# Optimization experiments

Hardware: AMD Instinct MI355X
Metric: run time of the kernel (lower is better)

## Reference

```python
import jax, jax.numpy as jnp
import numpy as np

HEAD_SIZE = 256
N_EMBS = 1024
B, T = 8, 2048


def setup_inputs() -> dict:
    key = jax.random.key(0)
    kx, kq, kk, kv = jax.random.split(key, 4)
    # nn.Linear default init: U(-1/sqrt(fan_in), 1/sqrt(fan_in)); weights stored [out, in],
    # we store transposed [in, out] for x @ W.
    bound = 1.0 / np.sqrt(N_EMBS)
    x = jax.random.normal(kx, (B, T, N_EMBS), dtype=jnp.float32)
    Wq = jax.random.uniform(kq, (N_EMBS, HEAD_SIZE), dtype=jnp.float32, minval=-bound, maxval=bound)
    Wk = jax.random.uniform(kk, (N_EMBS, HEAD_SIZE), dtype=jnp.float32, minval=-bound, maxval=bound)
    Wv = jax.random.uniform(kv, (N_EMBS, HEAD_SIZE), dtype=jnp.float32, minval=-bound, maxval=bound)
    return {"x": x, "Wq": Wq, "Wk": Wk, "Wv": Wv}


def reference(x, Wq, Wk, Wv):
    # x: [B, T, C]
    Bn, Tn, C = x.shape
    Q = x @ Wq  # [B, T, H]
    K = x @ Wk
    V = x @ Wv
    scale = 1.0 / jnp.sqrt(jnp.asarray(HEAD_SIZE, dtype=x.dtype))
    w = jnp.einsum("bth,bsh->bts", Q, K) * scale  # [B, T, T]
    causal = jnp.tril(jnp.ones((Tn, Tn), dtype=bool))
    w = jnp.where(causal, w, -jnp.inf)
    w = jax.nn.softmax(w, axis=-1)
    out = jnp.einsum("bts,bsh->bth", w, V)  # [B, T, H]
    return out
```

## Files before the change

### kernel.cpp

```cpp
#include <hip/hip_runtime.h>

typedef short short8 __attribute__((ext_vector_type(8)));
typedef short short4v __attribute__((ext_vector_type(4)));
typedef float floatx4 __attribute__((ext_vector_type(4)));

#define HEAD 256
#define CDIM 1024
#define TT   2048

#define NBLK 61

#define WT_EL    0
#define QW_EL    786560
#define KW_EL    (QW_EL + 4194304)
#define VT_EL    (KW_EL + 4194304)
#define XC_EL    (VT_EL + 4194304)
#define NEED_FULL_BYTES ((size_t)(XC_EL + 16777216) * 2)

static __device__ __forceinline__ unsigned short f2bf(float f) {
    unsigned int u = __builtin_bit_cast(unsigned int, f);
    u += 0x7FFFu + ((u >> 16) & 1u);
    return (unsigned short)(u >> 16);
}
static __device__ __forceinline__ float bf2f(unsigned short h) {
    unsigned int u = ((unsigned int)h) << 16;
    return __builtin_bit_cast(float, u);
}

__device__ __forceinline__ void glds16(const void* g, void* l) {
    __builtin_amdgcn_global_load_lds(
        (const __attribute__((address_space(1))) void*)g,
        (__attribute__((address_space(3))) void*)l, 16, 0, 0);
}

__device__ __forceinline__ int probe_f32(const unsigned short* Wq, int flat_tid) {
    int lane = flat_tid & 63;
    int bad = 0;
    for (int i = lane; i < 512; i += 64)
        bad |= (((Wq[i] >> 7) & 0xFF) >= 128) ? 1 : 0;
#pragma unroll
    for (int off = 1; off < 64; off <<= 1) bad |= __shfl_xor(bad, off);
    return bad;
}

__global__ __launch_bounds__(256) void prep_kernel(
    const void* __restrict__ x, unsigned short* __restrict__ XT,
    const void* __restrict__ Wq, const void* __restrict__ Wk,
    const void* __restrict__ Wv, unsigned short* __restrict__ WtT) {
    __shared__ unsigned short tile[32][33];
    int t = threadIdx.x;
    int f = probe_f32((const unsigned short*)Wq, t);
    if (blockIdx.x < 16384) {
        int row = blockIdx.x;
        int c4  = t * 4;
        size_t si = (size_t)row * CDIM + c4;
        size_t di = (size_t)(row >> 7) * 131072 + (size_t)(c4 >> 6) * 8192
                  + (size_t)(row & 127) * 64 + (c4 & 63);
        short4v o;
        if (f) {
            floatx4 v = *(const floatx4*)((const float*)x + si);
#pragma unroll
            for (int j = 0; j < 4; j++) o[j] = (short)f2bf(v[j]);
        } else {
            o = *(const short4v*)((const unsigned short*)x + si);
        }
        *(short4v*)&XT[di] = o;
    } else {
        int wid = blockIdx.x - 16384;
        int k0 = (wid & 31) * 32;
        int n0 = (wid >> 5) * 32;
        const void* W = (n0 < 256) ? Wq : (n0 < 512) ? Wk : Wv;
        int c0 = n0 & 255;
        int tx = t & 31, ty = t >> 5;
#pragma unroll
        for (int i = 0; i < 4; i++) {
            int r = ty + 8 * i;
            size_t idx = (size_t)(k0 + r) * HEAD + c0 + tx;
            tile[r][tx] = f ? f2bf(((const float*)W)[idx])
                            : ((const unsigned short*)W)[idx];
        }
        __syncthreads();
#pragma unroll
        for (int i = 0; i < 4; i++) {
            int n = n0 + ty + 8 * i;
            int k = k0 + tx;
            WtT[(size_t)(n >> 7) * 131072 + (size_t)(k >> 6) * 8192
                + (n & 127) * 64 + (k & 63)] = tile[tx][ty + 8 * i];
        }
    }
}

__global__ __launch_bounds__(256) void gemm_qkv(
    const unsigned short* __restrict__ XT,
    const unsigned short* __restrict__ WtT,
    unsigned short* __restrict__ Q,
    unsigned short* __restrict__ K,
    unsigned short* __restrict__ VT2) {
    __shared__ __attribute__((aligned(16))) short sh[16384];

    int tid  = threadIdx.x;
    int wave = tid >> 6, lane = tid & 63, quad = lane >> 4, lq = lane & 15;
    int wm = wave >> 1, wn = wave & 1;

    int id = blockIdx.x;
    int xcd = id & 7, g = id >> 3;
    int bn = g % 6;
    int bm = (g / 6) * 8 + xcd;
    int m0 = bm * 128, n0b = bn * 128;

    int l4 = lane >> 2;
    int cswz = ((lane & 3) ^ (l4 & 3) ^ ((l4 >> 2) & 3)) * 8;
    const unsigned short* gA = XT  + (size_t)bm * 131072
                               + (size_t)(wave * 32 + l4) * 64 + cswz;
    const unsigned short* gB = WtT + (size_t)bn * 131072
                               + (size_t)(wave * 32 + l4) * 64 + cswz;
    int rdswz = ((quad ^ (lq & 3) ^ ((lq >> 2) & 3))) * 8;

    floatx4 acc[4][4];
#pragma unroll
    for (int i = 0; i < 4; i++)
#pragma unroll
        for (int j = 0; j < 4; j++)
#pragma unroll
            for (int r = 0; r < 4; r++) acc[i][j][r] = 0.f;

    {
        short* dA = sh + wave * 1024;
        short* dB = sh + 4096 + wave * 1024;
        glds16(gA, dA); glds16(gA + 1024, dA + 512);
        glds16(gB, dB); glds16(gB + 1024, dB + 512);
    }

    int cur = 0;
    for (int s = 0; s < 32; s++) {
        __syncthreads();
        if (s + 1 < 32) {
            size_t off = (size_t)((s + 1) >> 1) * 8192 + ((s + 1) & 1) * 32;
            short* dA = sh + (cur ^ 1) * 8192 + wave * 1024;
            short* dB = sh + (cur ^ 1) * 8192 + 4096 + wave * 1024;
            glds16(gA + off, dA); glds16(gA + off + 1024, dA + 512);
            glds16(gB + off, dB); glds16(gB + off + 1024, dB + 512);
        }
        short* As_ = sh + cur * 8192;
        short* Bs_ = As_ + 4096;
        short8 af[4], bfv[4];
#pragma unroll
        for (int i = 0; i < 4; i++)
            af[i] = *(short8*)&As_[(64 * wm + 16 * i + lq) * 32 + rdswz];
#pragma unroll
        for (int j = 0; j < 4; j++)
            bfv[j] = *(short8*)&Bs_[(64 * wn + 16 * j + lq) * 32 + rdswz];
#pragma unroll
        for (int i = 0; i < 4; i++)
#pragma unroll
            for (int j = 0; j < 4; j++)
                acc[i][j] = __builtin_amdgcn_mfma_f32_16x16x32_bf16(
                    af[i], bfv[j], acc[i][j], 0, 0, 0);
        cur ^= 1;
    }

    int sel = n0b >> 8;
    if (sel < 2) {
        unsigned short* outp = (sel == 0) ? Q : K;
        float scale = (sel == 0) ? 0.0625f : 1.0f;
        int cbase = n0b & 255;
#pragma unroll
        for (int i = 0; i < 4; i++)
#pragma unroll
            for (int j = 0; j < 4; j++)
#pragma unroll
                for (int r = 0; r < 4; r++) {
                    int rr = m0 + 64 * wm + 16 * i + quad * 4 + r;
                    int cc = cbase + 64 * wn + 16 * j + lq;
                    outp[(size_t)rr * HEAD + cc] = f2bf(acc[i][j][r] * scale);
                }
    } else {
        int cbase = n0b - 512;
        int batch = m0 >> 11;
        int t0 = m0 & 2047;
        unsigned short* Vb = VT2 + (size_t)batch * HEAD * TT;
#pragma unroll
        for (int h = 0; h < 2; h++) {
            __syncthreads();
            if (wn == h) {
#pragma unroll
                for (int i = 0; i < 4; i++)
#pragma unroll
                    for (int j = 0; j < 4; j++)
#pragma unroll
                        for (int r = 0; r < 4; r++) {
                            int cl = 16 * j + lq;
                            int ml = 64 * wm + 16 * i + quad * 4 + r;
                            sh[cl * 136 + ml] = (short)f2bf(acc[i][j][r]);
                        }
            }
            __syncthreads();
            int cl = tid >> 2;
            int d = cbase + 64 * h + cl;
#pragma unroll
            for (int g2 = 0; g2 < 4; g2++) {
                int ms = (tid & 3) * 8 + g2 * 32;
                short8 v = *(short8*)&sh[cl * 136 + ms];
                int st = (t0 + ms) >> 5;
                int sc = ms & 31;
                *(short8*)&Vb[(size_t)st * 8192 + d * 32 + sc] = v;
            }
        }
    }
}

__global__ __launch_bounds__(256, 2) void attn(
    const unsigned short* __restrict__ Q,
    const unsigned short* __restrict__ K,
    const unsigned short* __restrict__ VT2,
    float* __restrict__ out,
    unsigned short* __restrict__ pO, float* __restrict__ pL) {
    __shared__ __attribute__((aligned(16))) short lds[37888];

    int tid  = threadIdx.x;
    int wave = tid >> 6, lane = tid & 63, quad = lane >> 4, lq = lane & 15;
    int b = blockIdx.x;
    int j = blockIdx.y;

    int qt, ci = 0, nch = 1, acc = 0;
    if (pO == nullptr) {
        qt = j;
    } else {
        int jr = NBLK - 1 - j;
        qt = 0;
        for (;;) {
            int n = (4 * qt + 13) / 10;
            if (jr < acc + n) { ci = jr - acc; nch = n; break; }
            acc += n; qt++;
        }
    }
    int T = 4 * qt + 4;
    int t_lo, t_hi;
    if (pO == nullptr) { t_lo = 0; t_hi = T; }
    else {
        int cb = T / nch, rem = T % nch;
        t_lo = ci * cb + min(ci, rem);
        t_hi = t_lo + cb + (ci < rem ? 1 : 0);
    }
    bool direct = (nch == 1);

    int q0 = qt * 128;
    size_t boff = (size_t)b * TT * HEAD;
    const unsigned short* Qb = Q + boff;
    const unsigned short* Kb = K + boff;
    const unsigned short* Vg = VT2 + boff;

    short8 qf[2][8];
#pragma unroll
    for (int i = 0; i < 2; i++) {
        int qrow = q0 + 32 * wave + 16 * i + lq;
#pragma unroll
        for (int kk = 0; kk < 8; kk++)
            qf[i][kk] = *(const short8*)&Qb[(size_t)qrow * HEAD + kk * 32 + quad * 8];
    }

    float l_part[2][4];
    floatx4 accO[2][16];
#pragma unroll
    for (int i = 0; i < 2; i++) {
#pragma unroll
        for (int r = 0; r < 4; r++) l_part[i][r] = 0.f;
#pragma unroll
        for (int n = 0; n < 16; n++)
#pragma unroll
            for (int r = 0; r < 4; r++) accO[i][n][r] = 0.f;
    }

    short* Ps = lds + 32768;

#define STAGE(buf, t_) do {                                                  \
        short* kd = lds + (buf) * 8192 + (4 * wave) * 512;                   \
        short* vd = lds + 16384 + (buf) * 8192 + (4 * wave) * 512;           \
        _Pragma("unroll")                                                    \
        for (int g = 0; g < 4; g++) {                                        \
            int row = 2 * (4 * wave + g) + (lane >> 5);                      \
            glds16(Kb + ((size_t)(t_) * 32 + row) * 256                      \
                       + (((lane & 31) ^ (row & 7)) << 3), kd + g * 512);    \
            glds16(Vg + (size_t)(t_) * 8192 + (size_t)(4 * wave + g) * 512   \
                       + lane * 8, vd + g * 512);                            \
        }                                                                    \
    } while (0)

    STAGE(0, t_lo);
    int cur = 0;
    for (int it = t_lo; it < t_hi; it++) {
        __syncthreads();
        if (it + 1 < t_hi) STAGE(cur ^ 1, it + 1);

        const short* Kt = lds + cur * 8192;
        const short* Vt = lds + 16384 + cur * 8192;

        floatx4 accS[2][2];
#pragma unroll
        for (int i = 0; i < 2; i++)
#pragma unroll
            for (int n = 0; n < 2; n++)
#pragma unroll
                for (int r = 0; r < 4; r++) accS[i][n][r] = 0.f;
#pragma unroll
        for (int kk = 0; kk < 8; kk++) {
            short8 bk[2];
#pragma unroll
            for (int n = 0; n < 2; n++)
                bk[n] = *(const short8*)&Kt[(16 * n + lq) * 256
                        + (((kk * 4 + quad) ^ (lq & 7)) << 3)];
#pragma unroll
            for (int i = 0; i < 2; i++)
#pragma unroll
                for (int n = 0; n < 2; n++)
                    accS[i][n] = __builtin_amdgcn_mfma_f32_16x16x32_bf16(
                        qf[i][kk], bk[n], accS[i][n], 0, 0, 0);
        }

        if (it >= 4 * qt) {
            int s0m = it * 32;
#pragma unroll
            for (int i = 0; i < 2; i++)
#pragma unroll
                for (int n = 0; n < 2; n++) {
                    int sg = s0m + 16 * n + lq;
#pragma unroll
                    for (int r = 0; r < 4; r++) {
                        int qg = q0 + 32 * wave + 16 * i + quad * 4 + r;
                        if (sg > qg) accS[i][n][r] = -1e30f;
                    }
                }
        }

#pragma unroll
        for (int i = 0; i < 2; i++)
#pragma unroll
            for (int n = 0; n < 2; n++)
#pragma unroll
                for (int r = 0; r < 4; r++) {
                    float pv = __expf(accS[i][n][r] - 8.0f);
                    l_part[i][r] += pv;
                    Ps[(32 * wave + 16 * i + quad * 4 + r) * 40 + 16 * n + lq] =
                        (short)f2bf(pv);
                }

        short8 ap0 = *(short8*)&Ps[(32 * wave + lq) * 40 + quad * 8];
        short8 ap1 = *(short8*)&Ps[(32 * wave + 16 + lq) * 40 + quad * 8];
#pragma unroll
        for (int n = 0; n < 16; n++) {
            short8 bv = *(const short8*)&Vt[(16 * n + lq) * 32 + quad * 8];
            accO[0][n] = __builtin_amdgcn_mfma_f32_16x16x32_bf16(ap0, bv, accO[0][n], 0, 0, 0);
            accO[1][n] = __builtin_amdgcn_mfma_f32_16x16x32_bf16(ap1, bv, accO[1][n], 0, 0, 0);
        }
        cur ^= 1;
    }
#undef STAGE

#pragma unroll
    for (int i = 0; i < 2; i++)
#pragma unroll
        for (int r = 0; r < 4; r++)
#pragma unroll
            for (int off = 1; off < 16; off <<= 1)
                l_part[i][r] += __shfl_xor(l_part[i][r], off);

    if (direct) {
        float* ob = out + boff;
#pragma unroll
        for (int i = 0; i < 2; i++)
#pragma unroll
            for (int r = 0; r < 4; r++) {
                float inv = 1.0f / l_part[i][r];
                int rr = q0 + 32 * wave + 16 * i + quad * 4 + r;
#pragma unroll
                for (int n = 0; n < 16; n++)
                    ob[(size_t)rr * HEAD + 16 * n + lq] = accO[i][n][r] * inv;
            }
    } else {
        int sidx = b * NBLK + acc + ci;
        unsigned short* po = pO + (size_t)sidx * 32768;
        if (lq == 0) {
#pragma unroll
            for (int i = 0; i < 2; i++)
#pragma unroll
                for (int r = 0; r < 4; r++)
                    pL[sidx * 128 + 32 * wave + 16 * i + quad * 4 + r] =
                        l_part[i][r];
        }
        __syncthreads();
        short* Ob = lds;
#pragma unroll
        for (int i = 0; i < 2; i++)
#pragma unroll
            for (int r = 0; r < 4; r++) {
                int rl = 32 * wave + 16 * i + quad * 4 + r;
#pragma unroll
                for (int n = 0; n < 16; n++)
                    Ob[rl * 256 + (((2 * n + (lq >> 3)) ^ (rl & 31)) << 3)
                       + (lq & 7)] = (short)f2bf(accO[i][n][r]);
            }
        __syncthreads();
        int c0 = tid & 3;
#pragma unroll
        for (int h = 0; h < 2; h++) {
            int row = (tid >> 2) + 64 * h;
#pragma unroll
            for (int g = 0; g < 8; g++) {
                int c = c0 | (g << 2);
                short8 v = *(short8*)&Ob[row * 256 + ((c ^ (row & 31)) << 3)];
                *(short8*)&po[row * 256 + (c << 3)] = v;
            }
        }
    }
}

__global__ __launch_bounds__(256) void reduce_attn(
    const unsigned short* __restrict__ pO, const float* __restrict__ pL,
    float* __restrict__ out) {
    int b = blockIdx.y, qt = 2 + blockIdx.x, rg = blockIdx.z;
    int pre = 2;
    for (int k = 2; k < qt; k++) pre += (4 * k + 13) / 10;
    int nch = (4 * qt + 13) / 10;
    int base = b * NBLK + pre;
    int tid = threadIdx.x;
    __shared__ float ls[16];
    if (tid < 16) {
        float s = 0.f;
        for (int c = 0; c < nch; c++)
            s += pL[(base + c) * 128 + rg * 16 + tid];
        ls[tid] = s;
    }
    __syncthreads();
    float* ob = out + (size_t)b * TT * HEAD
              + (size_t)(qt * 128 + rg * 16) * HEAD;
    for (int i = tid; i < 512; i += 256) {
        int row = i >> 5, c8 = (i & 31) * 8;
        float a[8];
#pragma unroll
        for (int k = 0; k < 8; k++) a[k] = 0.f;
        for (int c = 0; c < nch; c++) {
            short8 v = *(const short8*)&pO[(size_t)(base + c) * 32768
                        + (rg * 16 + row) * 256 + c8];
#pragma unroll
            for (int k = 0; k < 8; k++)
                a[k] += bf2f((unsigned short)v[k]);
        }
        float inv = 1.0f / ls[row];
#pragma unroll
        for (int k = 0; k < 8; k++)
            ob[(size_t)row * HEAD + c8 + k] = a[k] * inv;
    }
}

extern "C" void kernel_launch(void* const* d_in, const int* in_sizes, int n_in,
                              void* d_out, int out_size, void* d_ws, size_t ws_size,
                              hipStream_t stream) {
    const void* x  = d_in[0];
    const void* Wq = d_in[1];
    const void* Wk = d_in[2];
    const void* Wv = d_in[3];
    unsigned short* ws = (unsigned short*)d_ws;

    unsigned short* WtT = ws + WT_EL;
    unsigned short* Qw  = ws + QW_EL;
    unsigned short* Kw  = ws + KW_EL;
    unsigned short* VT2 = ws + VT_EL;
    unsigned short* xc  = ws + XC_EL;
    float* outp = (float*)d_out;

    bool full = (ws_size >= NEED_FULL_BYTES);

    const unsigned short* Xp;
    if (full) {
        prep_kernel<<<17152, 256, 0, stream>>>(x, xc, Wq, Wk, Wv, WtT);
        Xp = xc;
    } else {
        prep_kernel<<<dim3(768), 256, 0, stream>>>(x, xc, Wq, Wk, Wv, WtT);
        Xp = (const unsigned short*)x;
    }

    gemm_qkv<<<768, 256, 0, stream>>>(Xp, WtT, Qw, Kw, VT2);

    if (full) {
        unsigned short* pO = xc;
        float* pL = (float*)(ws + WT_EL);
        attn<<<dim3(8, NBLK), 256, 0, stream>>>(Qw, Kw, VT2, outp, pO, pL);
        reduce_attn<<<dim3(14, 8, 8), 256, 0, stream>>>(pO, pL, outp);
    } else {
        attn<<<dim3(8, 16), 256, 0, stream>>>(Qw, Kw, VT2, outp,
                                              (unsigned short*)nullptr,
                                              (float*)nullptr);
    }
}
```

Baseline: 204.5 us.

## Fuse split-KV reduction into attention kernel via last-block atomic counter

Removes the separate reduce_attn launch. Each attention block bumps a per-(batch, query-tile) atomic counter after writing its partial output, and the last block to arrive sums the partial outputs and normalizers and writes the final result. This saves one kernel launch and its dependency gap, but adds a memset launch and serializes the reduction onto one block per tile, where the old reduce kernel spread it over 8 blocks. The counter region is placed inside the workspace, which may overlap the pL buffer at WT_EL.

```diff
diff --git a/kernel.cpp b/kernel.cpp
--- a/kernel.cpp
+++ b/kernel.cpp
@@ -11,6 +11,7 @@
 #define NBLK 61
 
 #define WT_EL    0
+#define CTR_EL   262144
 #define QW_EL    786560
 #define KW_EL    (QW_EL + 4194304)
 #define VT_EL    (KW_EL + 4194304)
@@ -214,8 +215,10 @@
     const unsigned short* __restrict__ K,
     const unsigned short* __restrict__ VT2,
     float* __restrict__ out,
-    unsigned short* __restrict__ pO, float* __restrict__ pL) {
+    unsigned short* __restrict__ pO, float* __restrict__ pL,
+    int* __restrict__ ctr) {
     __shared__ __attribute__((aligned(16))) short lds[37888];
+    __shared__ int lastflag;
 
     int tid  = threadIdx.x;
     int wave = tid >> 6, lane = tid & 63, quad = lane >> 4, lq = lane & 15;
@@ -411,44 +414,42 @@
                 *(short8*)&po[row * 256 + (c << 3)] = v;
             }
         }
-    }
-}
-
-__global__ __launch_bounds__(256) void reduce_attn(
-    const unsigned short* __restrict__ pO, const float* __restrict__ pL,
-    float* __restrict__ out) {
-    int b = blockIdx.y, qt = 2 + blockIdx.x, rg = blockIdx.z;
-    int pre = 2;
-    for (int k = 2; k < qt; k++) pre += (4 * k + 13) / 10;
-    int nch = (4 * qt + 13) / 10;
-    int base = b * NBLK + pre;
-    int tid = threadIdx.x;
-    __shared__ float ls[16];
-    if (tid < 16) {
-        float s = 0.f;
-        for (int c = 0; c < nch; c++)
-            s += pL[(base + c) * 128 + rg * 16 + tid];
-        ls[tid] = s;
-    }
-    __syncthreads();
-    float* ob = out + (size_t)b * TT * HEAD
-              + (size_t)(qt * 128 + rg * 16) * HEAD;
-    for (int i = tid; i < 512; i += 256) {
-        int row = i >> 5, c8 = (i & 31) * 8;
-        float a[8];
-#pragma unroll
-        for (int k = 0; k < 8; k++) a[k] = 0.f;
-        for (int c = 0; c < nch; c++) {
-            short8 v = *(const short8*)&pO[(size_t)(base + c) * 32768
-                        + (rg * 16 + row) * 256 + c8];
-#pragma unroll
-            for (int k = 0; k < 8; k++)
-                a[k] += bf2f((unsigned short)v[k]);
-        }
-        float inv = 1.0f / ls[row];
-#pragma unroll
-        for (int k = 0; k < 8; k++)
-            ob[(size_t)row * HEAD + c8 + k] = a[k] * inv;
+
+        __threadfence();
+        __syncthreads();
+        if (tid == 0)
+            lastflag = atomicAdd(&ctr[b * 16 + qt], 1);
+        __syncthreads();
+        if (lastflag == nch - 1) {
+            __threadfence();
+            float* lsf = (float*)lds;
+            int base = b * NBLK + acc;
+            if (tid < 128) {
+                float s = 0.f;
+                for (int c = 0; c < nch; c++)
+                    s += pL[(base + c) * 128 + tid];
+                lsf[tid] = s;
+            }
+            __syncthreads();
+            float* ob = out + boff + (size_t)q0 * HEAD;
+            for (int i = tid; i < 4096; i += 256) {
+                int row = i >> 5, c8 = (i & 31) * 8;
+                float a[8];
+#pragma unroll
+                for (int k = 0; k < 8; k++) a[k] = 0.f;
+                for (int c = 0; c < nch; c++) {
+                    short8 v = *(const short8*)&pO[(size_t)(base + c) * 32768
+                                                   + row * 256 + c8];
+#pragma unroll
+                    for (int k = 0; k < 8; k++)
+                        a[k] += bf2f((unsigned short)v[k]);
+                }
+                float inv = 1.0f / lsf[row];
+#pragma unroll
+                for (int k = 0; k < 8; k++)
+                    ob[(size_t)row * HEAD + c8 + k] = a[k] * inv;
+            }
+        }
     }
 }
 
@@ -484,11 +485,13 @@
     if (full) {
         unsigned short* pO = xc;
         float* pL = (float*)(ws + WT_EL);
-        attn<<<dim3(8, NBLK), 256, 0, stream>>>(Qw, Kw, VT2, outp, pO, pL);
-        reduce_attn<<<dim3(14, 8, 8), 256, 0, stream>>>(pO, pL, outp);
+        int* ctr  = (int*)(ws + CTR_EL);
+        hipMemsetAsync(ctr, 0, 128 * sizeof(int), stream);
+        attn<<<dim3(8, NBLK), 256, 0, stream>>>(Qw, Kw, VT2, outp, pO, pL, ctr);
     } else {
         attn<<<dim3(8, 16), 256, 0, stream>>>(Qw, Kw, VT2, outp,
                                               (unsigned short*)nullptr,
-                                              (float*)nullptr);
-    }
-}
+                                              (float*)nullptr,
+                                              (int*)nullptr);
+    }
+}
```

New measurement: 316.5 us. +54.8%, slower.
